# Optimization experiments

Hardware: AMD Instinct MI355X
Metric: run time of the kernel (lower is better)

## Reference

```python
import jax, jax.numpy as jnp
import numpy as np
from itertools import permutations

# NOTE: the original torch code has `loss_m = loss_r = loss_i = []`, so all three
# names alias ONE list; RI_loss = 2*sum(L) and Mag_loss = sum(L), giving a total
# of 3*sum(per-speaker r+i+mag losses)/num_spks. We reproduce that factor of 3.

def reference(masks, mixture_real, mixture_imag, target_real, target_imag, input_sizes):
    S, B, M, W, F, T, _ = masks.shape
    filt = jax.lax.complex(masks[..., 0], masks[..., 1])          # [S,B,M,W,F,T]
    mix = jax.lax.complex(mixture_real, mixture_imag)             # [S,B,M,F,T]
    ref_ch = 0
    tgt = jax.lax.complex(target_real[:, :, ref_ch], target_imag[:, :, ref_ch])  # [S,B,F,T]

    # filtering(): unfold W time-shifted copies (zero padded) then MAC over (m,w)
    p = (W - 1) // 2
    mix_pad = jnp.pad(mix, ((0, 0), (0, 0), (0, 0), (0, 0), (p, p)))
    win = jnp.stack([mix_pad[..., w:w + T] for w in range(W)], axis=3)  # [S,B,M,W,F,T]
    out = jnp.einsum('sbmwft,sbmwft->sbft', win, filt)            # [S,B,F,T] complex

    # filtering output is permutation-invariant: build pairwise loss matrix once
    d = tgt[None, :] - out[:, None]                               # [S_out, S_tgt, B, F, T]
    lr = jnp.sum(jnp.abs(d.real), axis=(-1, -2))                  # [S,S,B]
    li = jnp.sum(jnp.abs(d.imag), axis=(-1, -2))
    lm = jnp.sum(jnp.abs(jnp.abs(tgt[None, :]) - jnp.abs(out[:, None])), axis=(-1, -2))
    L = lr + li + lm                                              # [S,S,B]

    perms = list(permutations(range(S)))
    pscore = jnp.stack([3.0 * sum(L[s, pm[s]] for s in range(S)) / S for pm in perms])  # [P,B]
    min_perutt = jnp.min(pscore, axis=0)                          # [B]
    num_utts = input_sizes.shape[0]
    return jnp.sum(min_perutt) / num_utts


def setup_inputs() -> dict:
    key = jax.random.key(0)
    ks = jax.random.split(key, 6)
    S, B, M, W, F, T, C = 2, 4, 4, 3, 257, 512, 4
    masks = jax.random.normal(ks[0], (S, B, M, W, F, T, 2), dtype=jnp.float32)
    mixture_real = jax.random.normal(ks[1], (S, B, M, F, T), dtype=jnp.float32)
    mixture_imag = jax.random.normal(ks[2], (S, B, M, F, T), dtype=jnp.float32)
    target_real = jax.random.normal(ks[3], (S, B, C, F, T), dtype=jnp.float32)
    target_imag = jax.random.normal(ks[4], (S, B, C, F, T), dtype=jnp.float32)
    input_sizes = jax.random.randint(ks[5], (B,), 1, 512).astype(jnp.int64)
    return {"masks": masks, "mixture_real": mixture_real, "mixture_imag": mixture_imag,
            "target_real": target_real, "target_imag": target_imag, "input_sizes": input_sizes}
```

## Files before the change

kernel.cpp:

```cpp
#include <hip/hip_runtime.h>

#define S_SPK 2
#define B_BATCH 4
#define M_MIC 4
#define W_TAP 3
#define F_FREQ 257
#define T_TIME 512
#define C_CH 4
#define FT (F_FREQ * T_TIME)


__global__ void zero_ws_kernel(float* ws) {
    if (threadIdx.x < 16) ws[threadIdx.x] = 0.0f;
}

__global__ __launch_bounds__(128) void pit_main_kernel(
    const float* __restrict__ masks,
    const float* __restrict__ mixr,
    const float* __restrict__ mixi,
    const float* __restrict__ tgtr,
    const float* __restrict__ tgti,
    float* __restrict__ ws)
{
    const int sb   = blockIdx.y;
    const int so   = sb / B_BATCH;
    const int b    = sb % B_BATCH;
    const int wave = threadIdx.x >> 6;
    const int lane = threadIdx.x & 63;
    const int f    = blockIdx.x * 2 + wave;
    const int t0   = lane * 8;

    float L0 = 0.0f, L1 = 0.0f;

    if (f < F_FREQ) {
        float orr[8], oii[8];
        #pragma unroll
        for (int j = 0; j < 8; ++j) { orr[j] = 0.0f; oii[j] = 0.0f; }

        const int ft       = f * T_TIME + t0;
        const int mixBase  = sb * M_MIC * FT;
        const int mskBase  = sb * M_MIC * W_TAP * FT * 2;

        #pragma unroll
        for (int m = 0; m < M_MIC; ++m) {
            const float* mrp = mixr + mixBase + m * FT + ft;
            const float* mip = mixi + mixBase + m * FT + ft;

            float rwin[10], iwin[10];
            {
                const float4 ra = *(const float4*)(mrp);
                const float4 rb = *(const float4*)(mrp + 4);
                const float4 ia = *(const float4*)(mip);
                const float4 ib = *(const float4*)(mip + 4);
                rwin[0] = (t0 > 0) ? mrp[-1] : 0.0f;
                iwin[0] = (t0 > 0) ? mip[-1] : 0.0f;
                rwin[1] = ra.x; rwin[2] = ra.y; rwin[3] = ra.z; rwin[4] = ra.w;
                rwin[5] = rb.x; rwin[6] = rb.y; rwin[7] = rb.z; rwin[8] = rb.w;
                iwin[1] = ia.x; iwin[2] = ia.y; iwin[3] = ia.z; iwin[4] = ia.w;
                iwin[5] = ib.x; iwin[6] = ib.y; iwin[7] = ib.z; iwin[8] = ib.w;
                rwin[9] = (t0 + 8 < T_TIME) ? mrp[8] : 0.0f;
                iwin[9] = (t0 + 8 < T_TIME) ? mip[8] : 0.0f;
            }

            #pragma unroll
            for (int w = 0; w < W_TAP; ++w) {
                const float4* mp = (const float4*)(masks + mskBase + (m * W_TAP + w) * FT * 2 + ft * 2);
                #pragma unroll
                for (int k = 0; k < 4; ++k) {
                    const float4 fl = mp[k];
                    const int j0 = 2 * k, j1 = 2 * k + 1;
                    orr[j0] += rwin[j0 + w] * fl.x - iwin[j0 + w] * fl.y;
                    oii[j0] += rwin[j0 + w] * fl.y + iwin[j0 + w] * fl.x;
                    orr[j1] += rwin[j1 + w] * fl.z - iwin[j1 + w] * fl.w;
                    oii[j1] += rwin[j1 + w] * fl.w + iwin[j1 + w] * fl.z;
                }
            }
        }

        #pragma unroll
        for (int st = 0; st < S_SPK; ++st) {
            const int tBase = (st * B_BATCH + b) * C_CH * FT + ft;
            const float4 tra = *(const float4*)(tgtr + tBase);
            const float4 trb = *(const float4*)(tgtr + tBase + 4);
            const float4 tia = *(const float4*)(tgti + tBase);
            const float4 tib = *(const float4*)(tgti + tBase + 4);
            const float tr[8] = {tra.x, tra.y, tra.z, tra.w, trb.x, trb.y, trb.z, trb.w};
            const float ti[8] = {tia.x, tia.y, tia.z, tia.w, tib.x, tib.y, tib.z, tib.w};
            float acc = 0.0f;
            #pragma unroll
            for (int j = 0; j < 8; ++j) {
                const float ao = sqrtf(orr[j] * orr[j] + oii[j] * oii[j]);
                const float at = sqrtf(tr[j] * tr[j] + ti[j] * ti[j]);
                acc += fabsf(tr[j] - orr[j]) + fabsf(ti[j] - oii[j]) + fabsf(at - ao);
            }
            if (st == 0) L0 = acc; else L1 = acc;
        }
    }

    #pragma unroll
    for (int off = 32; off > 0; off >>= 1) {
        L0 += __shfl_down(L0, off, 64);
        L1 += __shfl_down(L1, off, 64);
    }
    __shared__ float s0[2], s1[2];
    if (lane == 0) { s0[wave] = L0; s1[wave] = L1; }
    __syncthreads();
    if (threadIdx.x == 0) {
        atomicAdd(&ws[(so * S_SPK + 0) * B_BATCH + b], s0[0] + s0[1]);
        atomicAdd(&ws[(so * S_SPK + 1) * B_BATCH + b], s1[0] + s1[1]);
    }
}

__global__ void pit_final_kernel(const float* __restrict__ ws,
                                 float* __restrict__ out, int num_utts) {
    if (threadIdx.x == 0 && blockIdx.x == 0) {
        float acc = 0.0f;
        for (int b = 0; b < B_BATCH; ++b) {
            const float pid = ws[(0 * S_SPK + 0) * B_BATCH + b] + ws[(1 * S_SPK + 1) * B_BATCH + b];
            const float psw = ws[(0 * S_SPK + 1) * B_BATCH + b] + ws[(1 * S_SPK + 0) * B_BATCH + b];
            const float sc0 = 3.0f * pid / (float)S_SPK;
            const float sc1 = 3.0f * psw / (float)S_SPK;
            acc += fminf(sc0, sc1);
        }
        out[0] = acc / (float)num_utts;
    }
}

extern "C" void kernel_launch(void* const* d_in, const int* in_sizes, int n_in,
                              void* d_out, int out_size, void* d_ws, size_t ws_size,
                              hipStream_t stream) {
    const float* masks = (const float*)d_in[0];
    const float* mixr  = (const float*)d_in[1];
    const float* mixi  = (const float*)d_in[2];
    const float* tgtr  = (const float*)d_in[3];
    const float* tgti  = (const float*)d_in[4];
    const int num_utts = in_sizes[5];

    float* ws  = (float*)d_ws;
    float* out = (float*)d_out;

    zero_ws_kernel<<<1, 64, 0, stream>>>(ws);

    dim3 grid((F_FREQ + 1) / 2, S_SPK * B_BATCH);
    pit_main_kernel<<<grid, 128, 0, stream>>>(masks, mixr, mixi, tgtr, tgti, ws);

    pit_final_kernel<<<1, 64, 0, stream>>>(ws, out, num_utts);
}
```

Before: 219.3 us.

## Stage mask rows into LDS via async global_load_lds with one frequency per block

Each block now handles one frequency row with 256 threads, each computing two time steps. The 12 mask rows (M*W taps) are copied into shared memory with direct global-to-LDS async loads, while the mixture and target loads are issued during the copy. This is meant to improve memory-level parallelism and coalescing on a bandwidth-bound kernel. In exchange it adds 48KB of LDS per block, which limits occupancy, plus a barrier before compute. It also makes redundant overlapping mixture loads, since each thread reads a four-element window for two outputs.

```diff
diff --git a/kernel.cpp b/kernel.cpp
--- a/kernel.cpp
+++ b/kernel.cpp
@@ -8,13 +8,21 @@
 #define T_TIME 512
 #define C_CH 4
 #define FT (F_FREQ * T_TIME)
+#define MW (M_MIC * W_TAP)
+#define ROW (T_TIME * 2)
 
+__device__ __forceinline__ void async_copy16(const float* g, float* l) {
+    __builtin_amdgcn_global_load_lds(
+        (const __attribute__((address_space(1))) void*)g,
+        (__attribute__((address_space(3))) void*)l,
+        16, 0, 0);
+}
 
 __global__ void zero_ws_kernel(float* ws) {
     if (threadIdx.x < 16) ws[threadIdx.x] = 0.0f;
 }
 
-__global__ __launch_bounds__(128) void pit_main_kernel(
+__global__ __launch_bounds__(256) void pit_main_kernel(
     const float* __restrict__ masks,
     const float* __restrict__ mixr,
     const float* __restrict__ mixi,
@@ -22,79 +30,89 @@
     const float* __restrict__ tgti,
     float* __restrict__ ws)
 {
+    __shared__ float maskLDS[MW * ROW];
+    __shared__ float s0[4], s1[4];
+
     const int sb   = blockIdx.y;
     const int so   = sb / B_BATCH;
     const int b    = sb % B_BATCH;
-    const int wave = threadIdx.x >> 6;
-    const int lane = threadIdx.x & 63;
-    const int f    = blockIdx.x * 2 + wave;
-    const int t0   = lane * 8;
+    const int f    = blockIdx.x;
+    const int tid  = threadIdx.x;
+    const int wave = tid >> 6;
+    const int lane = tid & 63;
 
-    float L0 = 0.0f, L1 = 0.0f;
+    {
+        const long mskBase = (long)sb * MW * (FT * 2L) + (long)f * ROW;
+        #pragma unroll
+        for (int j = 0; j < 12; ++j) {
+            const int inst = wave * 12 + j;
+            const int row  = inst >> 2;
+            const int seg  = inst & 3;
+            const float* g = masks + mskBase + (long)row * (FT * 2L) + seg * 256 + lane * 4;
+            float*       l = maskLDS + row * ROW + seg * 256 + lane * 4;
+            async_copy16(g, l);
+        }
+    }
 
-    if (f < F_FREQ) {
-        float orr[8], oii[8];
-        #pragma unroll
-        for (int j = 0; j < 8; ++j) { orr[j] = 0.0f; oii[j] = 0.0f; }
-
-        const int ft       = f * T_TIME + t0;
-        const int mixBase  = sb * M_MIC * FT;
-        const int mskBase  = sb * M_MIC * W_TAP * FT * 2;
-
+    const int t0 = tid * 2;
+    float mr[M_MIC][4], mi[M_MIC][4];
+    {
+        const long mixBase = (long)sb * M_MIC * (long)FT + (long)f * T_TIME + t0;
         #pragma unroll
         for (int m = 0; m < M_MIC; ++m) {
-            const float* mrp = mixr + mixBase + m * FT + ft;
-            const float* mip = mixi + mixBase + m * FT + ft;
-
-            float rwin[10], iwin[10];
-            {
-                const float4 ra = *(const float4*)(mrp);
-                const float4 rb = *(const float4*)(mrp + 4);
-                const float4 ia = *(const float4*)(mip);
-                const float4 ib = *(const float4*)(mip + 4);
-                rwin[0] = (t0 > 0) ? mrp[-1] : 0.0f;
-                iwin[0] = (t0 > 0) ? mip[-1] : 0.0f;
-                rwin[1] = ra.x; rwin[2] = ra.y; rwin[3] = ra.z; rwin[4] = ra.w;
-                rwin[5] = rb.x; rwin[6] = rb.y; rwin[7] = rb.z; rwin[8] = rb.w;
-                iwin[1] = ia.x; iwin[2] = ia.y; iwin[3] = ia.z; iwin[4] = ia.w;
-                iwin[5] = ib.x; iwin[6] = ib.y; iwin[7] = ib.z; iwin[8] = ib.w;
-                rwin[9] = (t0 + 8 < T_TIME) ? mrp[8] : 0.0f;
-                iwin[9] = (t0 + 8 < T_TIME) ? mip[8] : 0.0f;
-            }
-
-            #pragma unroll
-            for (int w = 0; w < W_TAP; ++w) {
-                const float4* mp = (const float4*)(masks + mskBase + (m * W_TAP + w) * FT * 2 + ft * 2);
-                #pragma unroll
-                for (int k = 0; k < 4; ++k) {
-                    const float4 fl = mp[k];
-                    const int j0 = 2 * k, j1 = 2 * k + 1;
-                    orr[j0] += rwin[j0 + w] * fl.x - iwin[j0 + w] * fl.y;
-                    oii[j0] += rwin[j0 + w] * fl.y + iwin[j0 + w] * fl.x;
-                    orr[j1] += rwin[j1 + w] * fl.z - iwin[j1 + w] * fl.w;
-                    oii[j1] += rwin[j1 + w] * fl.w + iwin[j1 + w] * fl.z;
-                }
-            }
+            const float* mrp = mixr + mixBase + (long)m * FT;
+            const float* mip = mixi + mixBase + (long)m * FT;
+            const int km = (t0 > 0) ? -1 : 0;
+            const int kp = (t0 + 2 < T_TIME) ? 2 : 1;
+            float r0 = mrp[km], i0 = mip[km];
+            float r3 = mrp[kp], i3 = mip[kp];
+            mr[m][0] = (t0 > 0) ? r0 : 0.0f;
+            mi[m][0] = (t0 > 0) ? i0 : 0.0f;
+            mr[m][1] = mrp[0];  mi[m][1] = mip[0];
+            mr[m][2] = mrp[1];  mi[m][2] = mip[1];
+            mr[m][3] = (t0 + 2 < T_TIME) ? r3 : 0.0f;
+            mi[m][3] = (t0 + 2 < T_TIME) ? i3 : 0.0f;
         }
-
+    }
+    float2 tr[2], ti[2];
+    {
         #pragma unroll
         for (int st = 0; st < S_SPK; ++st) {
-            const int tBase = (st * B_BATCH + b) * C_CH * FT + ft;
-            const float4 tra = *(const float4*)(tgtr + tBase);
-            const float4 trb = *(const float4*)(tgtr + tBase + 4);
-            const float4 tia = *(const float4*)(tgti + tBase);
-            const float4 tib = *(const float4*)(tgti + tBase + 4);
-            const float tr[8] = {tra.x, tra.y, tra.z, tra.w, trb.x, trb.y, trb.z, trb.w};
-            const float ti[8] = {tia.x, tia.y, tia.z, tia.w, tib.x, tib.y, tib.z, tib.w};
-            float acc = 0.0f;
-            #pragma unroll
-            for (int j = 0; j < 8; ++j) {
-                const float ao = sqrtf(orr[j] * orr[j] + oii[j] * oii[j]);
-                const float at = sqrtf(tr[j] * tr[j] + ti[j] * ti[j]);
-                acc += fabsf(tr[j] - orr[j]) + fabsf(ti[j] - oii[j]) + fabsf(at - ao);
-            }
-            if (st == 0) L0 = acc; else L1 = acc;
+            const long tB = ((long)(st * B_BATCH + b) * C_CH) * FT + (long)f * T_TIME + t0;
+            tr[st] = *(const float2*)(tgtr + tB);
+            ti[st] = *(const float2*)(tgti + tB);
         }
+    }
+
+    __syncthreads();
+
+    float or0 = 0.f, oi0 = 0.f, or1 = 0.f, oi1 = 0.f;
+    #pragma unroll
+    for (int m = 0; m < M_MIC; ++m) {
+        #pragma unroll
+        for (int w = 0; w < W_TAP; ++w) {
+            const float4 fl = *(const float4*)(maskLDS + (m * W_TAP + w) * ROW + t0 * 2);
+            const float wr0 = mr[m][w],     wi0 = mi[m][w];
+            const float wr1 = mr[m][w + 1], wi1 = mi[m][w + 1];
+            or0 += wr0 * fl.x - wi0 * fl.y;
+            oi0 += wr0 * fl.y + wi0 * fl.x;
+            or1 += wr1 * fl.z - wi1 * fl.w;
+            oi1 += wr1 * fl.w + wi1 * fl.z;
+        }
+    }
+
+    float L0, L1;
+    {
+        const float ao0 = sqrtf(or0 * or0 + oi0 * oi0);
+        const float ao1 = sqrtf(or1 * or1 + oi1 * oi1);
+        const float at00 = sqrtf(tr[0].x * tr[0].x + ti[0].x * ti[0].x);
+        const float at01 = sqrtf(tr[0].y * tr[0].y + ti[0].y * ti[0].y);
+        const float at10 = sqrtf(tr[1].x * tr[1].x + ti[1].x * ti[1].x);
+        const float at11 = sqrtf(tr[1].y * tr[1].y + ti[1].y * ti[1].y);
+        L0 = fabsf(tr[0].x - or0) + fabsf(ti[0].x - oi0) + fabsf(at00 - ao0)
+           + fabsf(tr[0].y - or1) + fabsf(ti[0].y - oi1) + fabsf(at01 - ao1);
+        L1 = fabsf(tr[1].x - or0) + fabsf(ti[1].x - oi0) + fabsf(at10 - ao0)
+           + fabsf(tr[1].y - or1) + fabsf(ti[1].y - oi1) + fabsf(at11 - ao1);
     }
 
     #pragma unroll
@@ -102,12 +120,11 @@
         L0 += __shfl_down(L0, off, 64);
         L1 += __shfl_down(L1, off, 64);
     }
-    __shared__ float s0[2], s1[2];
     if (lane == 0) { s0[wave] = L0; s1[wave] = L1; }
     __syncthreads();
-    if (threadIdx.x == 0) {
-        atomicAdd(&ws[(so * S_SPK + 0) * B_BATCH + b], s0[0] + s0[1]);
-        atomicAdd(&ws[(so * S_SPK + 1) * B_BATCH + b], s1[0] + s1[1]);
+    if (tid == 0) {
+        atomicAdd(&ws[(so * S_SPK + 0) * B_BATCH + b], s0[0] + s0[1] + s0[2] + s0[3]);
+        atomicAdd(&ws[(so * S_SPK + 1) * B_BATCH + b], s1[0] + s1[1] + s1[2] + s1[3]);
     }
 }
 
@@ -141,8 +158,8 @@
 
     zero_ws_kernel<<<1, 64, 0, stream>>>(ws);
 
-    dim3 grid((F_FREQ + 1) / 2, S_SPK * B_BATCH);
-    pit_main_kernel<<<grid, 128, 0, stream>>>(masks, mixr, mixi, tgtr, tgti, ws);
+    dim3 grid(F_FREQ, S_SPK * B_BATCH);
+    pit_main_kernel<<<grid, 256, 0, stream>>>(masks, mixr, mixi, tgtr, tgti, ws);
 
     pit_final_kernel<<<1, 64, 0, stream>>>(ws, out, num_utts);
 }
```

New measurement: 213.7 us. 1.03x faster.

## Halve per-thread work, use 256-thread blocks, nontemporal mask loads

Applied to the files above, without the earlier changes.

Each thread now handles 4 time samples instead of 8, with four waves per block covering two frequency rows in two halves. Block size doubles so more threads are in flight for this memory-bound kernel. Mask reads use nontemporal loads because the masks are streamed once. The shared-memory block reduction is replaced by per-wave atomics, which doubles the number of atomics and adds more edge loads per output sample.

```diff
diff --git a/kernel.cpp b/kernel.cpp
--- a/kernel.cpp
+++ b/kernel.cpp
@@ -10,11 +10,17 @@
 #define FT (F_FREQ * T_TIME)
 
 
+typedef float floatx4 __attribute__((ext_vector_type(4)));
+
 __global__ void zero_ws_kernel(float* ws) {
     if (threadIdx.x < 16) ws[threadIdx.x] = 0.0f;
 }
 
-__global__ __launch_bounds__(128) void pit_main_kernel(
+__device__ __forceinline__ floatx4 nt_load4(const float* p) {
+    return __builtin_nontemporal_load((const floatx4*)p);
+}
+
+__global__ __launch_bounds__(256) void pit_main_kernel(
     const float* __restrict__ masks,
     const float* __restrict__ mixr,
     const float* __restrict__ mixi,
@@ -27,71 +33,68 @@
     const int b    = sb % B_BATCH;
     const int wave = threadIdx.x >> 6;
     const int lane = threadIdx.x & 63;
-    const int f    = blockIdx.x * 2 + wave;
-    const int t0   = lane * 8;
+    const int f    = blockIdx.x * 2 + (wave >> 1);
+    const int t0   = (wave & 1) * 256 + lane * 4;
 
     float L0 = 0.0f, L1 = 0.0f;
 
     if (f < F_FREQ) {
-        float orr[8], oii[8];
-        #pragma unroll
-        for (int j = 0; j < 8; ++j) { orr[j] = 0.0f; oii[j] = 0.0f; }
+        float orr[4] = {0.f, 0.f, 0.f, 0.f};
+        float oii[4] = {0.f, 0.f, 0.f, 0.f};
 
-        const int ft       = f * T_TIME + t0;
-        const int mixBase  = sb * M_MIC * FT;
-        const int mskBase  = sb * M_MIC * W_TAP * FT * 2;
+        const int ft      = f * T_TIME + t0;
+        const int mixBase = sb * M_MIC * FT + ft;
+        const int mskBase = (sb * M_MIC * W_TAP) * (FT * 2) + ft * 2;
+        const bool lo_ok  = (t0 > 0);
+        const bool hi_ok  = (t0 + 4 < T_TIME);
 
-        #pragma unroll
+        #pragma unroll 1
         for (int m = 0; m < M_MIC; ++m) {
-            const float* mrp = mixr + mixBase + m * FT + ft;
-            const float* mip = mixi + mixBase + m * FT + ft;
+            const float* mrp = mixr + mixBase + m * FT;
+            const float* mip = mixi + mixBase + m * FT;
 
-            float rwin[10], iwin[10];
+            float wr[6], wi[6];
             {
-                const float4 ra = *(const float4*)(mrp);
-                const float4 rb = *(const float4*)(mrp + 4);
-                const float4 ia = *(const float4*)(mip);
-                const float4 ib = *(const float4*)(mip + 4);
-                rwin[0] = (t0 > 0) ? mrp[-1] : 0.0f;
-                iwin[0] = (t0 > 0) ? mip[-1] : 0.0f;
-                rwin[1] = ra.x; rwin[2] = ra.y; rwin[3] = ra.z; rwin[4] = ra.w;
-                rwin[5] = rb.x; rwin[6] = rb.y; rwin[7] = rb.z; rwin[8] = rb.w;
-                iwin[1] = ia.x; iwin[2] = ia.y; iwin[3] = ia.z; iwin[4] = ia.w;
-                iwin[5] = ib.x; iwin[6] = ib.y; iwin[7] = ib.z; iwin[8] = ib.w;
-                rwin[9] = (t0 + 8 < T_TIME) ? mrp[8] : 0.0f;
-                iwin[9] = (t0 + 8 < T_TIME) ? mip[8] : 0.0f;
+                const float4 r4 = *(const float4*)mrp;
+                const float4 i4 = *(const float4*)mip;
+                wr[0] = lo_ok ? mrp[-1] : 0.0f;
+                wi[0] = lo_ok ? mip[-1] : 0.0f;
+                wr[1] = r4.x; wr[2] = r4.y; wr[3] = r4.z; wr[4] = r4.w;
+                wi[1] = i4.x; wi[2] = i4.y; wi[3] = i4.z; wi[4] = i4.w;
+                wr[5] = hi_ok ? mrp[4] : 0.0f;
+                wi[5] = hi_ok ? mip[4] : 0.0f;
             }
 
+            const int mB = mskBase + (m * W_TAP) * (FT * 2);
             #pragma unroll
             for (int w = 0; w < W_TAP; ++w) {
-                const float4* mp = (const float4*)(masks + mskBase + (m * W_TAP + w) * FT * 2 + ft * 2);
-                #pragma unroll
-                for (int k = 0; k < 4; ++k) {
-                    const float4 fl = mp[k];
-                    const int j0 = 2 * k, j1 = 2 * k + 1;
-                    orr[j0] += rwin[j0 + w] * fl.x - iwin[j0 + w] * fl.y;
-                    oii[j0] += rwin[j0 + w] * fl.y + iwin[j0 + w] * fl.x;
-                    orr[j1] += rwin[j1 + w] * fl.z - iwin[j1 + w] * fl.w;
-                    oii[j1] += rwin[j1 + w] * fl.w + iwin[j1 + w] * fl.z;
-                }
+                const float* mp = masks + mB + w * (FT * 2);
+                const floatx4 f0 = nt_load4(mp);
+                const floatx4 f1 = nt_load4(mp + 4);
+                orr[0] += wr[w]     * f0.x - wi[w]     * f0.y;
+                oii[0] += wr[w]     * f0.y + wi[w]     * f0.x;
+                orr[1] += wr[w + 1] * f0.z - wi[w + 1] * f0.w;
+                oii[1] += wr[w + 1] * f0.w + wi[w + 1] * f0.z;
+                orr[2] += wr[w + 2] * f1.x - wi[w + 2] * f1.y;
+                oii[2] += wr[w + 2] * f1.y + wi[w + 2] * f1.x;
+                orr[3] += wr[w + 3] * f1.z - wi[w + 3] * f1.w;
+                oii[3] += wr[w + 3] * f1.w + wi[w + 3] * f1.z;
             }
         }
 
         #pragma unroll
         for (int st = 0; st < S_SPK; ++st) {
-            const int tBase = (st * B_BATCH + b) * C_CH * FT + ft;
-            const float4 tra = *(const float4*)(tgtr + tBase);
-            const float4 trb = *(const float4*)(tgtr + tBase + 4);
-            const float4 tia = *(const float4*)(tgti + tBase);
-            const float4 tib = *(const float4*)(tgti + tBase + 4);
-            const float tr[8] = {tra.x, tra.y, tra.z, tra.w, trb.x, trb.y, trb.z, trb.w};
-            const float ti[8] = {tia.x, tia.y, tia.z, tia.w, tib.x, tib.y, tib.z, tib.w};
+            const int tB = (st * B_BATCH + b) * C_CH * FT + ft;
+            const float4 tr = *(const float4*)(tgtr + tB);
+            const float4 ti = *(const float4*)(tgti + tB);
+            const float trj[4] = {tr.x, tr.y, tr.z, tr.w};
+            const float tij[4] = {ti.x, ti.y, ti.z, ti.w};
             float acc = 0.0f;
             #pragma unroll
-            for (int j = 0; j < 8; ++j) {
+            for (int j = 0; j < 4; ++j) {
                 const float ao = sqrtf(orr[j] * orr[j] + oii[j] * oii[j]);
-                const float at = sqrtf(tr[j] * tr[j] + ti[j] * ti[j]);
-                acc += fabsf(tr[j] - orr[j]) + fabsf(ti[j] - oii[j]) + fabsf(at - ao);
+                const float at = sqrtf(trj[j] * trj[j] + tij[j] * tij[j]);
+                acc += fabsf(trj[j] - orr[j]) + fabsf(tij[j] - oii[j]) + fabsf(at - ao);
             }
             if (st == 0) L0 = acc; else L1 = acc;
         }
@@ -102,12 +105,9 @@
         L0 += __shfl_down(L0, off, 64);
         L1 += __shfl_down(L1, off, 64);
     }
-    __shared__ float s0[2], s1[2];
-    if (lane == 0) { s0[wave] = L0; s1[wave] = L1; }
-    __syncthreads();
-    if (threadIdx.x == 0) {
-        atomicAdd(&ws[(so * S_SPK + 0) * B_BATCH + b], s0[0] + s0[1]);
-        atomicAdd(&ws[(so * S_SPK + 1) * B_BATCH + b], s1[0] + s1[1]);
+    if (lane == 0 && f < F_FREQ) {
+        atomicAdd(&ws[(so * S_SPK + 0) * B_BATCH + b], L0);
+        atomicAdd(&ws[(so * S_SPK + 1) * B_BATCH + b], L1);
     }
 }
 
@@ -142,7 +142,7 @@
     zero_ws_kernel<<<1, 64, 0, stream>>>(ws);
 
     dim3 grid((F_FREQ + 1) / 2, S_SPK * B_BATCH);
-    pit_main_kernel<<<grid, 128, 0, stream>>>(masks, mixr, mixi, tgtr, tgti, ws);
+    pit_main_kernel<<<grid, 256, 0, stream>>>(masks, mixr, mixi, tgtr, tgti, ws);
 
     pit_final_kernel<<<1, 64, 0, stream>>>(ws, out, num_utts);
 }
```

Result: slower. 284.7 us (+29.9%).
